# Performance work log

Measured on AMD Instinct MI355X. Metric: run time of the kernel, lower is better.

The kernel has to match this reference:

```python
import jax, jax.numpy as jnp
import numpy as np

D_OUT = 32
INPUT_LEN = 2048
NUM_EIGH = 32
K_U = 3
K_Y = 2


def _top_hankel_eigh(n, k):
    # Hankel matrix Z[i,j] = 2 / ((i+j)^3 - (i+j)) for i,j in 1..n
    i = np.arange(1, n + 1, dtype=np.float64)
    s = i[:, None] + i[None, :]
    Z = 2.0 / (s ** 3 - s)
    vals, vecs = np.linalg.eigh(Z)
    return (jnp.asarray(vals[-k:], dtype=jnp.float32),
            jnp.asarray(vecs[:, -k:], dtype=jnp.float32))


def setup_inputs() -> dict:
    key = jax.random.key(0)
    k1, k2, k3, k4 = jax.random.split(key, 4)
    B = 32
    inputs = jax.random.normal(k1, (B, INPUT_LEN, D_OUT), dtype=jnp.float32)
    eig_vals, eig_vecs = _top_hankel_eigh(INPUT_LEN, NUM_EIGH)
    m_u = jax.random.normal(k2, (D_OUT, D_OUT, K_U), dtype=jnp.float32) * 0.02
    m_phi = jax.random.normal(k3, (D_OUT * NUM_EIGH, D_OUT), dtype=jnp.float32) * 0.02
    m_y = jax.random.normal(k4, (D_OUT, K_Y, D_OUT), dtype=jnp.float32) * 0.02
    return {"inputs": inputs, "eig_vals": eig_vals, "eig_vecs": eig_vecs,
            "m_u": m_u, "m_phi": m_phi, "m_y": m_y}


def _spectral_conv(v, u):
    # Causal FFT convolution of each filter v[:,k] with each channel u[:,:,d].
    # v: (l, k), u: (b, l, d) -> (b, l, k, d)
    l = v.shape[0]
    n = 2 * l
    V = jnp.fft.rfft(v, n=n, axis=0)          # (nf, k)
    U = jnp.fft.rfft(u, n=n, axis=1)          # (b, nf, d)
    P = V[None, :, :, None] * U[:, :, None, :]  # (b, nf, k, d)
    return jnp.fft.irfft(P, n=n, axis=1)[:, :l]


def _compute_x_tilde(inputs, eig_vals, eig_vecs):
    b, l, d = inputs.shape
    x_tilde = _spectral_conv(eig_vecs, inputs)                  # (b, l, k, d)
    x_tilde = x_tilde * (eig_vals ** 0.25)[None, None, :, None]
    return x_tilde.reshape(b, l, -1)                            # (b, l, k*d)


def _compute_ar_x_preds(w, x):
    # w: (d_out, d_in, k), x: (b, l, d_in) -> (b, l, d_out)
    d_out, d_in, k = w.shape
    b, l, _ = x.shape
    o = jnp.einsum('oik,bli->bklo', w, x)                       # (b, k, l, d_out)
    shifts = jnp.arange(k)
    rolled = jax.vmap(lambda oi, s: jnp.roll(oi, s, axis=1),
                      in_axes=(1, 0), out_axes=1)(o, shifts)    # (b, k, l, d_out)
    mask = (jnp.arange(l)[None, :] >= shifts[:, None]).astype(x.dtype)  # (k, l)
    return jnp.sum(rolled * mask[None, :, :, None], axis=1)


def _compute_y_t(m_y, deltas):
    # m_y: (d_out, k_y, d_out), deltas: (b, l, d_out)
    # y_t = sum_{j<k_y} m_y[:, j] @ y_{t-1-j} + delta_t
    b, l, d = deltas.shape
    ky = m_y.shape[1]
    carry0 = jnp.zeros((b, ky, d), dtype=deltas.dtype)

    def step(carry, x):
        out = jnp.einsum('oki,bki->bo', m_y, carry) + x
        carry = jnp.roll(carry, 1, axis=1).at[:, 0].set(out)
        return carry, out

    _, ys = jax.lax.scan(step, carry0, jnp.swapaxes(deltas, 0, 1))
    return jnp.swapaxes(ys, 0, 1)


def reference(inputs, eig_vals, eig_vecs, m_u, m_phi, m_y):
    x_tilde = _compute_x_tilde(inputs, eig_vals, eig_vecs)
    delta_phi = x_tilde @ m_phi
    delta_ar_u = _compute_ar_x_preds(m_u, inputs)
    return _compute_y_t(m_y, delta_phi + delta_ar_u)
```

## Files before the change

kernel.cpp:

```cpp
#include <hip/hip_runtime.h>
#include <math.h>

#define L     2048
#define NFFT  4096
#define NH    2049
#define UST   2052
#define D     32
#define B     32
#define KU    3
#define CCH   64
#define NCH   32

__device__ __forceinline__ int PHY(int i) { return i + (i >> 5); }
__device__ __forceinline__ int REV4(int i) {
  int r2 = __brev(i) >> 20;
  return ((r2 & 0x555) << 1) | ((r2 >> 1) & 0x555);
}

__global__ void k_init_tw(float2* __restrict__ tw) {
  int j = blockIdx.x * blockDim.x + threadIdx.x;
  if (j < NFFT) {
    double ang = -2.0 * 3.14159265358979323846 * (double)j / (double)NFFT;
    tw[j] = make_float2((float)cos(ang), (float)sin(ang));
  }
}

__device__ void dif6(float* sre, float* sim, const float2* __restrict__ tw, int tid) {
  #pragma unroll
  for (int st = 0; st < 6; ++st) {
    const int shift = 10 - 2 * st;
    const int q = 1 << shift;
    const int r = 1 << (2 * st);
    #pragma unroll
    for (int h = 0; h < 2; ++h) {
      const int idx = tid + h * 512;
      const int j = idx & (q - 1);
      const int g = idx >> shift;
      const int i0 = (g << (shift + 2)) + j;
      const int p0 = PHY(i0), p1 = PHY(i0 + q), p2 = PHY(i0 + 2 * q), p3 = PHY(i0 + 3 * q);
      float ax = sre[p0], ay = sim[p0], bx = sre[p1], by = sim[p1];
      float cx = sre[p2], cy = sim[p2], dx = sre[p3], dy = sim[p3];
      float t0x = ax + cx, t0y = ay + cy, t1x = ax - cx, t1y = ay - cy;
      float t2x = bx + dx, t2y = by + dy, t3x = bx - dx, t3y = by - dy;
      float2 w1 = tw[j * r];
      float w2x = w1.x * w1.x - w1.y * w1.y, w2y = 2.f * w1.x * w1.y;
      float w3x = w2x * w1.x - w2y * w1.y, w3y = w2x * w1.y + w2y * w1.x;
      sre[p0] = t0x + t2x; sim[p0] = t0y + t2y;
      float u1x = t1x + t3y, u1y = t1y - t3x;
      sre[p1] = u1x * w1.x - u1y * w1.y; sim[p1] = u1x * w1.y + u1y * w1.x;
      float u2x = t0x - t2x, u2y = t0y - t2y;
      sre[p2] = u2x * w2x - u2y * w2y; sim[p2] = u2x * w2y + u2y * w2x;
      float u3x = t1x - t3y, u3y = t1y + t3x;
      sre[p3] = u3x * w3x - u3y * w3y; sim[p3] = u3x * w3y + u3y * w3x;
    }
    __syncthreads();
  }
}

__device__ void dit6(float* sre, float* sim, const float2* __restrict__ tw, int tid) {
  #pragma unroll
  for (int st = 0; st < 6; ++st) {
    const int shift = 2 * st;
    const int q = 1 << shift;
    const int r = 1 << (10 - 2 * st);
    #pragma unroll
    for (int h = 0; h < 2; ++h) {
      const int idx = tid + h * 512;
      const int j = idx & (q - 1);
      const int g = idx >> shift;
      const int i0 = (g << (shift + 2)) + j;
      const int p0 = PHY(i0), p1 = PHY(i0 + q), p2 = PHY(i0 + 2 * q), p3 = PHY(i0 + 3 * q);
      float ax = sre[p0], ay = sim[p0], bx = sre[p1], by = sim[p1];
      float cx = sre[p2], cy = sim[p2], dx = sre[p3], dy = sim[p3];
      float2 w1 = tw[j * r]; w1.y = -w1.y;
      float w2x = w1.x * w1.x - w1.y * w1.y, w2y = 2.f * w1.x * w1.y;
      float w3x = w2x * w1.x - w2y * w1.y, w3y = w2x * w1.y + w2y * w1.x;
      float bpx = bx * w1.x - by * w1.y, bpy = bx * w1.y + by * w1.x;
      float cpx = cx * w2x - cy * w2y,   cpy = cx * w2y + cy * w2x;
      float dpx = dx * w3x - dy * w3y,   dpy = dx * w3y + dy * w3x;
      float t0x = ax + cpx, t0y = ay + cpy, t1x = ax - cpx, t1y = ay - cpy;
      float t2x = bpx + dpx, t2y = bpy + dpy, t3x = bpx - dpx, t3y = bpy - dpy;
      sre[p0] = t0x + t2x; sim[p0] = t0y + t2y;
      sre[p1] = t1x - t3y; sim[p1] = t1y + t3x;
      sre[p2] = t0x - t2x; sim[p2] = t0y - t2y;
      sre[p3] = t1x + t3y; sim[p3] = t1y - t3x;
    }
    __syncthreads();
  }
}

__global__ __launch_bounds__(256) void k_tr(const float* __restrict__ u,
                                            float2* __restrict__ uTp) {
  __shared__ float tile[64][33];
  const int b = blockIdx.y;
  const int t0 = blockIdx.x * 64;
  const int tid = threadIdx.x;
  for (int i = tid; i < 64 * 32; i += 256) {
    int tl = i >> 5, d = i & 31;
    tile[tl][d] = u[((size_t)b * L + t0 + tl) * D + d];
  }
  __syncthreads();
  for (int i = tid; i < 16 * 64; i += 256) {
    int p = i >> 6, tt = i & 63;
    uTp[((size_t)b * 16 + p) * L + t0 + tt] =
        make_float2(tile[tt][2 * p], tile[tt][2 * p + 1]);
  }
}

__global__ __launch_bounds__(512) void k_fft_fwd(const float2* __restrict__ uTp,
                                                 const float* __restrict__ eig_vecs,
                                                 const float* __restrict__ eig_vals,
                                                 const float2* __restrict__ tw,
                                                 float2* __restrict__ Ubuf,
                                                 float2* __restrict__ Vf) {
  __shared__ float sre[4224];
  __shared__ float sim[4224];
  const int blk = blockIdx.x;
  const int tid = threadIdx.x;
  if (blk < 512) {
    const float2* zp = uTp + (size_t)blk * L;
    for (int t = tid; t < L; t += 512) {
      float2 z = zp[t];
      int p = PHY(t);
      sre[p] = z.x; sim[p] = z.y;
    }
  } else {
    const int p2 = blk - 512;
    for (int t = tid; t < L; t += 512) {
      int p = PHY(t);
      sre[p] = eig_vecs[(size_t)t * D + 2 * p2];
      sim[p] = eig_vecs[(size_t)t * D + 2 * p2 + 1];
    }
  }
  for (int t = L + tid; t < NFFT; t += 512) {
    int p = PHY(t);
    sre[p] = 0.f; sim[p] = 0.f;
  }
  __syncthreads();
  dif6(sre, sim, tw, tid);
  if (blk < 512) {
    float2* r0 = Ubuf + (size_t)(2 * blk) * UST;
    float2* r1 = r0 + UST;
    for (int f = tid; f <= 2048; f += 512) {
      int pa = PHY(REV4(f));
      int pc = PHY(REV4((NFFT - f) & (NFFT - 1)));
      float Ax = sre[pa], Ay = sim[pa];
      float Bx = sre[pc], By = -sim[pc];
      r0[f] = make_float2(0.5f * (Ax + Bx), 0.5f * (Ay + By));
      float Dx = Ax - Bx, Dy = Ay - By;
      r1[f] = make_float2(0.5f * Dy, -0.5f * Dx);
    }
  } else {
    const int p2 = blk - 512;
    const float sc0 = powf(eig_vals[2 * p2], 0.25f);
    const float sc1 = powf(eig_vals[2 * p2 + 1], 0.25f);
    float2* r0 = Vf + (size_t)(2 * p2) * UST;
    float2* r1 = r0 + UST;
    for (int f = tid; f <= 2048; f += 512) {
      int pa = PHY(REV4(f));
      int pc = PHY(REV4((NFFT - f) & (NFFT - 1)));
      float Ax = sre[pa], Ay = sim[pa];
      float Bx = sre[pc], By = -sim[pc];
      r0[f] = make_float2(0.5f * sc0 * (Ax + Bx), 0.5f * sc0 * (Ay + By));
      float Dx = Ax - Bx, Dy = Ay - By;
      r1[f] = make_float2(0.5f * sc1 * Dy, -0.5f * sc1 * Dx);
    }
  }
}

__global__ __launch_bounds__(1024) void k_w(const float2* __restrict__ Vf,
                                            const float* __restrict__ m_phi,
                                            float2* __restrict__ Wm) {
  __shared__ float2 vl[D];
  const int f = blockIdx.x, tid = threadIdx.x;
  if (tid < D) vl[tid] = Vf[(size_t)tid * UST + f];
  __syncthreads();
  const int d = tid >> 5, o = tid & 31;
  float2 acc = make_float2(0.f, 0.f);
  #pragma unroll
  for (int k = 0; k < D; ++k) {
    float m = m_phi[(k * D + d) * D + o];
    float2 v = vl[k];
    acc.x += v.x * m;
    acc.y += v.y * m;
  }
  Wm[(size_t)f * D * D + d * D + o] = acc;
}

#define FT 8
#define BC 8
__global__ __launch_bounds__(256) void k_mix(const float2* __restrict__ Ubuf,
                                             const float2* __restrict__ Wm,
                                             float2* __restrict__ Qbuf) {
  __shared__ float2 Ul[BC][D][FT];
  __shared__ float2 Qs[BC][D][FT];
  const int f0 = blockIdx.x * FT;
  const int tid = threadIdx.x;
  const int o = tid & 31, fi = tid >> 5;
  const int f = f0 + fi;
  float2 Wr[D];
  if (f < NH) {
    const float2* wp = Wm + (size_t)f * D * D + o;
    #pragma unroll
    for (int d = 0; d < D; ++d) Wr[d] = wp[d * D];
  } else {
    #pragma unroll
    for (int d = 0; d < D; ++d) Wr[d] = make_float2(0.f, 0.f);
  }
  const int lf = tid & 7, row = tid >> 3;
  for (int b0 = 0; b0 < B; b0 += BC) {
    #pragma unroll
    for (int it = 0; it < 8; ++it) {
      int r = row + it * 32;
      int bc = r >> 5, d = r & 31;
      int ff = f0 + lf;
      Ul[bc][d][lf] = (ff < NH)
          ? Ubuf[((size_t)(b0 + bc) * D + d) * UST + ff]
          : make_float2(0.f, 0.f);
    }
    __syncthreads();
    #pragma unroll
    for (int bc = 0; bc < BC; ++bc) {
      float ax = 0.f, ay = 0.f;
      #pragma unroll
      for (int d = 0; d < D; ++d) {
        float2 uu = Ul[bc][d][fi];
        float2 ww = Wr[d];
        ax += uu.x * ww.x - uu.y * ww.y;
        ay += uu.x * ww.y + uu.y * ww.x;
      }
      Qs[bc][o][(fi + o) & 7] = make_float2(ax, ay);
    }
    __syncthreads();
    #pragma unroll
    for (int it = 0; it < 8; ++it) {
      int r = row + it * 32;
      int bc = r >> 5, oo = r & 31;
      int ff = f0 + lf;
      if (ff < NH)
        Qbuf[((size_t)(b0 + bc) * D + oo) * UST + ff] = Qs[bc][oo][(lf + oo) & 7];
    }
    __syncthreads();
  }
}

__global__ __launch_bounds__(512) void k_ifft(const float2* __restrict__ Qbuf,
                                              const float2* __restrict__ tw,
                                              float* __restrict__ dT) {
  __shared__ float sre[4224];
  __shared__ float sim[4224];
  const int blk = blockIdx.x;
  const int tid = threadIdx.x;
  const float2* r0 = Qbuf + (size_t)(2 * blk) * UST;
  const float2* r1 = r0 + UST;
  for (int f = tid; f <= 2048; f += 512) {
    float2 q1 = r0[f], q2 = r1[f];
    int pa = PHY(REV4(f));
    int pc = PHY(REV4((NFFT - f) & (NFFT - 1)));
    sre[pa] = q1.x - q2.y; sim[pa] = q1.y + q2.x;
    sre[pc] = q1.x + q2.y; sim[pc] = -q1.y + q2.x;
  }
  __syncthreads();
  dit6(sre, sim, tw, tid);
  float* d0 = dT + (size_t)(2 * blk) * L;
  float* d1 = d0 + L;
  const float inv = 1.0f / (float)NFFT;
  for (int t = tid; t < L; t += 512) {
    int p = PHY(t);
    d0[t] = sre[p] * inv;
    d1[t] = sim[p] * inv;
  }
}

#define TT 64
__global__ __launch_bounds__(256) void k_ar(const float* __restrict__ dT,
                                            const float* __restrict__ u,
                                            const float* __restrict__ m_u,
                                            float* __restrict__ delta) {
  __shared__ float Ds[D][TT + 1];
  __shared__ float Us[TT + 2][D];
  __shared__ float Mt[KU][D][D];
  const int b = blockIdx.y;
  const int t0 = blockIdx.x * TT;
  const int tid = threadIdx.x;
  for (int idx = tid; idx < D * D * KU; idx += blockDim.x) {
    int k = idx % KU, i = (idx / KU) % D, o = idx / (KU * D);
    Mt[k][i][o] = m_u[idx];
  }
  for (int idx = tid; idx < D * TT; idx += blockDim.x) {
    int o = idx >> 6, tt = idx & 63;
    Ds[o][tt] = dT[((size_t)b * D + o) * L + t0 + tt];
  }
  for (int idx = tid; idx < (TT + 2) * D; idx += blockDim.x) {
    int j = idx >> 5, i = idx & 31;
    int t = t0 - 2 + j;
    Us[j][i] = (t >= 0) ? u[((size_t)b * L + t) * D + i] : 0.f;
  }
  __syncthreads();
  const int o = tid & 31, ts = tid >> 5;
  for (int tt = ts; tt < TT; tt += 8) {
    int t = t0 + tt;
    float acc = Ds[o][tt];
    #pragma unroll
    for (int k2 = 0; k2 < KU; ++k2) {
      if (t >= k2) {
        const float* ur = Us[tt + 2 - k2];
        #pragma unroll
        for (int i = 0; i < D; ++i) acc += Mt[k2][i][o] * ur[i];
      }
    }
    delta[((size_t)b * L + t) * D + o] = acc;
  }
}

__global__ __launch_bounds__(1024) void k_tc(const float* __restrict__ m_y,
                                             float* __restrict__ Tc) {
  __shared__ float A[64][68];
  __shared__ float Bb[64][68];
  const int tid = threadIdx.x;
  for (int idx = tid; idx < 64 * 64; idx += blockDim.x) {
    int r = idx >> 6, c = idx & 63;
    float v;
    if (r < 32) v = m_y[(r * 2 + (c >> 5)) * D + (c & 31)];
    else        v = (c == r - 32) ? 1.f : 0.f;
    A[r][c] = v;
  }
  __syncthreads();
  const int r = tid >> 4, cg = tid & 15;
  for (int it = 0; it < 6; ++it) {
    float4 acc = make_float4(0.f, 0.f, 0.f, 0.f);
    for (int i = 0; i < 64; ++i) {
      float a = A[r][i];
      float4 v = *(const float4*)&A[i][cg * 4];
      acc.x += a * v.x; acc.y += a * v.y; acc.z += a * v.z; acc.w += a * v.w;
    }
    __syncthreads();
    *(float4*)&Bb[r][cg * 4] = acc;
    __syncthreads();
    *(float4*)&A[r][cg * 4] = *(const float4*)&Bb[r][cg * 4];
    __syncthreads();
  }
  for (int idx = tid; idx < 64 * 64; idx += blockDim.x)
    Tc[idx] = A[idx >> 6][idx & 63];
}

__global__ void k_scanA(const float* __restrict__ delta,
                        const float* __restrict__ m_y,
                        float* __restrict__ shat) {
  __shared__ float yb[2][D];
  const int b = blockIdx.y, c = blockIdx.x;
  const int lane = threadIdx.x;
  const int o = lane & 31, h = lane >> 5;
  float m0[16], m1[16];
  #pragma unroll
  for (int i = 0; i < 16; ++i) {
    m0[i] = m_y[(o * 2 + 0) * D + h * 16 + i];
    m1[i] = m_y[(o * 2 + 1) * D + h * 16 + i];
  }
  if (lane < D) { yb[0][lane] = 0.f; yb[1][lane] = 0.f; }
  __syncthreads();
  const float* dp = delta + ((size_t)b * L + c * CCH) * D;
  float ylast = 0.f, yprev = 0.f;
  for (int r = 0; r < CCH; ++r) {
    const float* y1 = yb[(r + 1) & 1];
    const float* y2 = yb[r & 1];
    float acc = 0.f;
    #pragma unroll
    for (int i = 0; i < 16; ++i)
      acc += m0[i] * y1[h * 16 + i] + m1[i] * y2[h * 16 + i];
    acc += __shfl_xor(acc, 32);
    float y = acc + dp[r * D + o];
    __syncthreads();
    if (h == 0) yb[r & 1][o] = y;
    __syncthreads();
    yprev = ylast; ylast = y;
  }
  if (h == 0) {
    float* sp = shat + ((size_t)b * NCH + c) * 64;
    sp[o] = ylast;
    sp[32 + o] = yprev;
  }
}

__global__ void k_scanB(const float* __restrict__ Tc,
                        const float* __restrict__ shat,
                        float* __restrict__ sin_) {
  __shared__ float TcT[64][65];
  __shared__ float sb[64];
  const int b = blockIdx.x;
  const int r = threadIdx.x;
  for (int idx = r; idx < 64 * 64; idx += 64) {
    int rr = idx >> 6, cc = idx & 63;
    TcT[cc][rr] = Tc[idx];
  }
  sb[r] = 0.f;
  __syncthreads();
  for (int c = 0; c < NCH; ++c) {
    sin_[((size_t)b * NCH + c) * 64 + r] = sb[r];
    float acc = 0.f;
    #pragma unroll 8
    for (int i = 0; i < 64; ++i) acc += TcT[i][r] * sb[i];
    acc += shat[((size_t)b * NCH + c) * 64 + r];
    __syncthreads();
    sb[r] = acc;
    __syncthreads();
  }
}

__global__ void k_scanC(const float* __restrict__ delta,
                        const float* __restrict__ m_y,
                        const float* __restrict__ sin_,
                        float* __restrict__ out) {
  __shared__ float yb[2][D];
  const int b = blockIdx.y, c = blockIdx.x;
  const int lane = threadIdx.x;
  const int o = lane & 31, h = lane >> 5;
  float m0[16], m1[16];
  #pragma unroll
  for (int i = 0; i < 16; ++i) {
    m0[i] = m_y[(o * 2 + 0) * D + h * 16 + i];
    m1[i] = m_y[(o * 2 + 1) * D + h * 16 + i];
  }
  const float* sp = sin_ + ((size_t)b * NCH + c) * 64;
  if (lane < 32) yb[1][lane] = sp[lane];
  else           yb[0][lane - 32] = sp[lane];
  __syncthreads();
  const float* dp = delta + ((size_t)b * L + c * CCH) * D;
  float* op = out + ((size_t)b * L + c * CCH) * D;
  for (int r = 0; r < CCH; ++r) {
    const float* y1 = yb[(r + 1) & 1];
    const float* y2 = yb[r & 1];
    float acc = 0.f;
    #pragma unroll
    for (int i = 0; i < 16; ++i)
      acc += m0[i] * y1[h * 16 + i] + m1[i] * y2[h * 16 + i];
    acc += __shfl_xor(acc, 32);
    float y = acc + dp[r * D + o];
    __syncthreads();
    if (h == 0) { yb[r & 1][o] = y; op[r * D + o] = y; }
    __syncthreads();
  }
}

extern "C" void kernel_launch(void* const* d_in, const int* in_sizes, int n_in,
                              void* d_out, int out_size, void* d_ws, size_t ws_size,
                              hipStream_t stream) {
  const float* u        = (const float*)d_in[0];
  const float* eig_vals = (const float*)d_in[1];
  const float* eig_vecs = (const float*)d_in[2];
  const float* m_u      = (const float*)d_in[3];
  const float* m_phi    = (const float*)d_in[4];
  const float* m_y      = (const float*)d_in[5];
  float* out = (float*)d_out;

  char* ws = (char*)d_ws;
  size_t off = 0;
  auto alloc = [&](size_t bytes) -> void* {
    void* p = ws + off;
    off += bytes;
    off = (off + 255) & ~(size_t)255;
    return p;
  };
  float2* tw   = (float2*)alloc((size_t)NFFT * sizeof(float2));
  float2* uTp  = (float2*)alloc((size_t)B * 16 * L * sizeof(float2));
  float2* Vf   = (float2*)alloc((size_t)D * UST * sizeof(float2));
  float2* Wm   = (float2*)alloc((size_t)NH * D * D * sizeof(float2));
  float2* Ubuf = (float2*)alloc((size_t)B * D * UST * sizeof(float2));
  float2* Qbuf = (float2*)alloc((size_t)B * D * UST * sizeof(float2));
  float*  Tc   = (float*)alloc(64 * 64 * sizeof(float));
  float*  shat = (float*)alloc((size_t)B * NCH * 64 * sizeof(float));
  float*  sinb = (float*)alloc((size_t)B * NCH * 64 * sizeof(float));
  float* dT    = (float*)uTp;
  float* delta = (float*)Ubuf;

  k_init_tw<<<16, 256, 0, stream>>>(tw);
  k_tr     <<<dim3(L / 64, B), 256, 0, stream>>>(u, uTp);
  k_fft_fwd<<<528, 512, 0, stream>>>(uTp, eig_vecs, eig_vals, tw, Ubuf, Vf);
  k_w      <<<NH, 1024, 0, stream>>>(Vf, m_phi, Wm);
  k_mix    <<<(NH + FT - 1) / FT, 256, 0, stream>>>(Ubuf, Wm, Qbuf);
  k_ifft   <<<B * 16, 512, 0, stream>>>(Qbuf, tw, dT);
  k_ar     <<<dim3(L / TT, B), 256, 0, stream>>>(dT, u, m_u, delta);
  k_tc     <<<1, 1024, 0, stream>>>(m_y, Tc);
  k_scanA  <<<dim3(NCH, B), 64, 0, stream>>>(delta, m_y, shat);
  k_scanB  <<<B, 64, 0, stream>>>(Tc, shat, sinb);
  k_scanC  <<<dim3(NCH, B), 64, 0, stream>>>(delta, m_y, sinb, out);
}
```

Before: 278.6 us.

## Fuse W computation into mix kernel, fold twiddle init into transpose, stage deltas

Removes the separate k_w kernel and its large Wm intermediate by computing the per-frequency W matrix inside k_mix from Vf and m_phi. Twiddle generation moves into extra blocks of the transpose kernel, which drops one launch. The scan kernels now preload their 64x32 delta chunk into shared memory with float4 loads, so the serial recurrence no longer waits on a global load each step. The cost is that each k_mix block recomputes W with many m_phi reads, adding register pressure and redundant arithmetic.

Result: faster. 271.1 us (-2.7%).

```diff
diff --git a/kernel.cpp b/kernel.cpp
--- a/kernel.cpp
+++ b/kernel.cpp
@@ -15,14 +15,6 @@
 __device__ __forceinline__ int REV4(int i) {
   int r2 = __brev(i) >> 20;
   return ((r2 & 0x555) << 1) | ((r2 >> 1) & 0x555);
-}
-
-__global__ void k_init_tw(float2* __restrict__ tw) {
-  int j = blockIdx.x * blockDim.x + threadIdx.x;
-  if (j < NFFT) {
-    double ang = -2.0 * 3.14159265358979323846 * (double)j / (double)NFFT;
-    tw[j] = make_float2((float)cos(ang), (float)sin(ang));
-  }
 }
 
 __device__ void dif6(float* sre, float* sim, const float2* __restrict__ tw, int tid) {
@@ -90,11 +82,23 @@
 }
 
 __global__ __launch_bounds__(256) void k_tr(const float* __restrict__ u,
-                                            float2* __restrict__ uTp) {
+                                            float2* __restrict__ uTp,
+                                            float2* __restrict__ tw) {
+  const int bx = blockIdx.x;
+  const int b = blockIdx.y;
+  const int tid = threadIdx.x;
+  if (bx >= L / 64) {
+    if (b == 0) {
+      for (int jj = tid; jj < 2048; jj += 256) {
+        int j = (bx - L / 64) * 2048 + jj;
+        double ang = -2.0 * 3.14159265358979323846 * (double)j / (double)NFFT;
+        tw[j] = make_float2((float)cos(ang), (float)sin(ang));
+      }
+    }
+    return;
+  }
   __shared__ float tile[64][33];
-  const int b = blockIdx.y;
-  const int t0 = blockIdx.x * 64;
-  const int tid = threadIdx.x;
+  const int t0 = bx * 64;
   for (int i = tid; i < 64 * 32; i += 256) {
     int tl = i >> 5, d = i & 31;
     tile[tl][d] = u[((size_t)b * L + t0 + tl) * D + d];
@@ -168,47 +172,42 @@
   }
 }
 
-__global__ __launch_bounds__(1024) void k_w(const float2* __restrict__ Vf,
-                                            const float* __restrict__ m_phi,
-                                            float2* __restrict__ Wm) {
-  __shared__ float2 vl[D];
-  const int f = blockIdx.x, tid = threadIdx.x;
-  if (tid < D) vl[tid] = Vf[(size_t)tid * UST + f];
-  __syncthreads();
-  const int d = tid >> 5, o = tid & 31;
-  float2 acc = make_float2(0.f, 0.f);
-  #pragma unroll
-  for (int k = 0; k < D; ++k) {
-    float m = m_phi[(k * D + d) * D + o];
-    float2 v = vl[k];
-    acc.x += v.x * m;
-    acc.y += v.y * m;
-  }
-  Wm[(size_t)f * D * D + d * D + o] = acc;
-}
-
 #define FT 8
 #define BC 8
 __global__ __launch_bounds__(256) void k_mix(const float2* __restrict__ Ubuf,
-                                             const float2* __restrict__ Wm,
+                                             const float2* __restrict__ Vf,
+                                             const float* __restrict__ m_phi,
                                              float2* __restrict__ Qbuf) {
   __shared__ float2 Ul[BC][D][FT];
   __shared__ float2 Qs[BC][D][FT];
+  __shared__ float2 Vl[D][FT];
   const int f0 = blockIdx.x * FT;
   const int tid = threadIdx.x;
   const int o = tid & 31, fi = tid >> 5;
   const int f = f0 + fi;
+  {
+    int k = tid >> 3, ff = tid & 7;
+    int fff = f0 + ff;
+    Vl[k][ff] = (fff < NH) ? Vf[(size_t)k * UST + fff] : make_float2(0.f, 0.f);
+  }
+  __syncthreads();
   float2 Wr[D];
-  if (f < NH) {
-    const float2* wp = Wm + (size_t)f * D * D + o;
-    #pragma unroll
-    for (int d = 0; d < D; ++d) Wr[d] = wp[d * D];
-  } else {
-    #pragma unroll
-    for (int d = 0; d < D; ++d) Wr[d] = make_float2(0.f, 0.f);
+  #pragma unroll
+  for (int d = 0; d < D; ++d) Wr[d] = make_float2(0.f, 0.f);
+  const float* mp = m_phi + o;
+  for (int k = 0; k < D; ++k) {
+    float2 v = Vl[k][fi];
+    const float* mk = mp + (size_t)k * D * D;
+    #pragma unroll
+    for (int d = 0; d < D; ++d) {
+      float m = mk[d * D];
+      Wr[d].x += v.x * m;
+      Wr[d].y += v.y * m;
+    }
   }
   const int lf = tid & 7, row = tid >> 3;
   for (int b0 = 0; b0 < B; b0 += BC) {
+    __syncthreads();
     #pragma unroll
     for (int it = 0; it < 8; ++it) {
       int r = row + it * 32;
@@ -240,7 +239,6 @@
       if (ff < NH)
         Qbuf[((size_t)(b0 + bc) * D + oo) * UST + ff] = Qs[bc][oo][(lf + oo) & 7];
     }
-    __syncthreads();
   }
 }
 
@@ -348,6 +346,7 @@
                         const float* __restrict__ m_y,
                         float* __restrict__ shat) {
   __shared__ float yb[2][D];
+  __shared__ float Dl[CCH][D + 1];
   const int b = blockIdx.y, c = blockIdx.x;
   const int lane = threadIdx.x;
   const int o = lane & 31, h = lane >> 5;
@@ -357,9 +356,16 @@
     m0[i] = m_y[(o * 2 + 0) * D + h * 16 + i];
     m1[i] = m_y[(o * 2 + 1) * D + h * 16 + i];
   }
+  const float* dp = delta + ((size_t)b * L + c * CCH) * D;
+  for (int j = lane; j < CCH * D / 4; j += 64) {
+    float4 v = ((const float4*)dp)[j];
+    int base = j * 4;
+    int r = base >> 5, col = base & 31;
+    Dl[r][col] = v.x; Dl[r][col + 1] = v.y;
+    Dl[r][col + 2] = v.z; Dl[r][col + 3] = v.w;
+  }
   if (lane < D) { yb[0][lane] = 0.f; yb[1][lane] = 0.f; }
   __syncthreads();
-  const float* dp = delta + ((size_t)b * L + c * CCH) * D;
   float ylast = 0.f, yprev = 0.f;
   for (int r = 0; r < CCH; ++r) {
     const float* y1 = yb[(r + 1) & 1];
@@ -369,7 +375,7 @@
     for (int i = 0; i < 16; ++i)
       acc += m0[i] * y1[h * 16 + i] + m1[i] * y2[h * 16 + i];
     acc += __shfl_xor(acc, 32);
-    float y = acc + dp[r * D + o];
+    float y = acc + Dl[r][o];
     __syncthreads();
     if (h == 0) yb[r & 1][o] = y;
     __syncthreads();
@@ -412,6 +418,7 @@
                         const float* __restrict__ sin_,
                         float* __restrict__ out) {
   __shared__ float yb[2][D];
+  __shared__ float Dl[CCH][D + 1];
   const int b = blockIdx.y, c = blockIdx.x;
   const int lane = threadIdx.x;
   const int o = lane & 31, h = lane >> 5;
@@ -421,11 +428,18 @@
     m0[i] = m_y[(o * 2 + 0) * D + h * 16 + i];
     m1[i] = m_y[(o * 2 + 1) * D + h * 16 + i];
   }
+  const float* dp = delta + ((size_t)b * L + c * CCH) * D;
+  for (int j = lane; j < CCH * D / 4; j += 64) {
+    float4 v = ((const float4*)dp)[j];
+    int base = j * 4;
+    int r = base >> 5, col = base & 31;
+    Dl[r][col] = v.x; Dl[r][col + 1] = v.y;
+    Dl[r][col + 2] = v.z; Dl[r][col + 3] = v.w;
+  }
   const float* sp = sin_ + ((size_t)b * NCH + c) * 64;
   if (lane < 32) yb[1][lane] = sp[lane];
   else           yb[0][lane - 32] = sp[lane];
   __syncthreads();
-  const float* dp = delta + ((size_t)b * L + c * CCH) * D;
   float* op = out + ((size_t)b * L + c * CCH) * D;
   for (int r = 0; r < CCH; ++r) {
     const float* y1 = yb[(r + 1) & 1];
@@ -435,7 +449,7 @@
     for (int i = 0; i < 16; ++i)
       acc += m0[i] * y1[h * 16 + i] + m1[i] * y2[h * 16 + i];
     acc += __shfl_xor(acc, 32);
-    float y = acc + dp[r * D + o];
+    float y = acc + Dl[r][o];
     __syncthreads();
     if (h == 0) { yb[r & 1][o] = y; op[r * D + o] = y; }
     __syncthreads();
@@ -464,7 +478,6 @@
   float2* tw   = (float2*)alloc((size_t)NFFT * sizeof(float2));
   float2* uTp  = (float2*)alloc((size_t)B * 16 * L * sizeof(float2));
   float2* Vf   = (float2*)alloc((size_t)D * UST * sizeof(float2));
-  float2* Wm   = (float2*)alloc((size_t)NH * D * D * sizeof(float2));
   float2* Ubuf = (float2*)alloc((size_t)B * D * UST * sizeof(float2));
   float2* Qbuf = (float2*)alloc((size_t)B * D * UST * sizeof(float2));
   float*  Tc   = (float*)alloc(64 * 64 * sizeof(float));
@@ -473,11 +486,9 @@
   float* dT    = (float*)uTp;
   float* delta = (float*)Ubuf;
 
-  k_init_tw<<<16, 256, 0, stream>>>(tw);
-  k_tr     <<<dim3(L / 64, B), 256, 0, stream>>>(u, uTp);
+  k_tr     <<<dim3(L / 64 + 2, B), 256, 0, stream>>>(u, uTp, tw);
   k_fft_fwd<<<528, 512, 0, stream>>>(uTp, eig_vecs, eig_vals, tw, Ubuf, Vf);
-  k_w      <<<NH, 1024, 0, stream>>>(Vf, m_phi, Wm);
-  k_mix    <<<(NH + FT - 1) / FT, 256, 0, stream>>>(Ubuf, Wm, Qbuf);
+  k_mix    <<<(NH + FT - 1) / FT, 256, 0, stream>>>(Ubuf, Vf, m_phi, Qbuf);
   k_ifft   <<<B * 16, 512, 0, stream>>>(Qbuf, tw, dT);
   k_ar     <<<dim3(L / TT, B), 256, 0, stream>>>(dT, u, m_u, delta);
   k_tc     <<<1, 1024, 0, stream>>>(m_y, Tc);
```
